# Performance work log

Hardware: AMD Instinct MI355X
Metric: run time of the kernel (lower is better)

The kernel has to match this reference:

```python
import jax, jax.numpy as jnp
import numpy as np

# Sparse MinkUNet-style backbone sizes
N0, N1, N2, N3 = 100000, 50000, 25000, 12500  # voxels per level (batch-concatenated)
K, KD = 27, 8        # 3x3x3 kernel offsets, stride-2 child offsets
B, S = 8, 1024       # batch, seed_num
C0, C1, C2, C3 = 32, 64, 128, 256
COUT = 512


def _w(k, shape, fan_in):
    return jax.random.normal(k, shape, dtype=jnp.float32) / np.sqrt(fan_in)


def setup_inputs() -> dict:
    key = jax.random.key(0)
    ks = jax.random.split(key, 32)
    inp = {}
    inp["feats"] = jax.random.normal(ks[0], (N0, 3), dtype=jnp.float32)
    # neighbor maps (kernel-offset gather indices, as built by a voxel hash map)
    inp["nbr0"] = jax.random.randint(ks[1], (N0, K), 0, N0, dtype=jnp.int32)
    inp["nbr1"] = jax.random.randint(ks[2], (N1, K), 0, N1, dtype=jnp.int32)
    inp["nbr2"] = jax.random.randint(ks[3], (N2, K), 0, N2, dtype=jnp.int32)
    inp["nbr3"] = jax.random.randint(ks[4], (N3, K), 0, N3, dtype=jnp.int32)
    # stride-2 downsample maps (coarse voxel -> fine children)
    inp["down1"] = jax.random.randint(ks[5], (N1, KD), 0, N0, dtype=jnp.int32)
    inp["down2"] = jax.random.randint(ks[6], (N2, KD), 0, N1, dtype=jnp.int32)
    inp["down3"] = jax.random.randint(ks[7], (N3, KD), 0, N2, dtype=jnp.int32)
    # nearest-parent upsample maps (fine voxel -> coarse parent)
    inp["up2"] = jax.random.randint(ks[8], (N2,), 0, N3, dtype=jnp.int32)
    inp["up1"] = jax.random.randint(ks[9], (N1,), 0, N2, dtype=jnp.int32)
    inp["up0"] = jax.random.randint(ks[10], (N0,), 0, N1, dtype=jnp.int32)
    # nearest-voxel devoxelize index for each FPS seed point
    inp["seed_idx"] = jax.random.randint(ks[11], (B, S), 0, N0, dtype=jnp.int32)
    # conv kernels [K, Cin, Cout] and 1x1 (linear) decoder weights
    inp["W_stem"] = _w(ks[12], (K, 3, C0), K * 3)
    inp["W_b0"] = _w(ks[13], (K, C0, C0), K * C0)
    inp["W_d1"] = _w(ks[14], (KD, C0, C1), KD * C0)
    inp["W_b1"] = _w(ks[15], (K, C1, C1), K * C1)
    inp["W_d2"] = _w(ks[16], (KD, C1, C2), KD * C1)
    inp["W_b2"] = _w(ks[17], (K, C2, C2), K * C2)
    inp["W_d3"] = _w(ks[18], (KD, C2, C3), KD * C2)
    inp["W_b3"] = _w(ks[19], (K, C3, C3), K * C3)
    inp["W_u2"] = _w(ks[20], (C3 + C2, 256), C3 + C2)
    inp["W_u1"] = _w(ks[21], (256 + C1, 128), 256 + C1)
    inp["W_u0"] = _w(ks[22], (128 + C0, 96), 128 + C0)
    inp["W_out"] = _w(ks[23], (96, COUT), 96)
    return inp


def sp_conv(f, nbr, W):
    # gather neighbor features then contract over (kernel offset, in-channel)
    g = f[nbr]                                # [N, K, Cin]
    return jnp.einsum('nkc,kco->no', g, W)    # [N, Cout]


def reference(feats, nbr0, nbr1, nbr2, nbr3, down1, down2, down3,
              up2, up1, up0, seed_idx,
              W_stem, W_b0, W_d1, W_b1, W_d2, W_b2, W_d3, W_b3,
              W_u2, W_u1, W_u0, W_out):
    relu = jax.nn.relu
    # encoder
    x0 = relu(sp_conv(feats, nbr0, W_stem))          # [N0, 32]
    x0 = x0 + relu(sp_conv(x0, nbr0, W_b0))
    x1 = relu(sp_conv(x0, down1, W_d1))              # [N1, 64]
    x1 = x1 + relu(sp_conv(x1, nbr1, W_b1))
    x2 = relu(sp_conv(x1, down2, W_d2))              # [N2, 128]
    x2 = x2 + relu(sp_conv(x2, nbr2, W_b2))
    x3 = relu(sp_conv(x2, down3, W_d3))              # [N3, 256]
    x3 = x3 + relu(sp_conv(x3, nbr3, W_b3))
    # decoder: nearest-parent upsample + skip concat + 1x1 conv
    u2 = relu(jnp.concatenate([x3[up2], x2], axis=-1) @ W_u2)   # [N2, 256]
    u1 = relu(jnp.concatenate([u2[up1], x1], axis=-1) @ W_u1)   # [N1, 128]
    u0 = relu(jnp.concatenate([u1[up0], x0], axis=-1) @ W_u0)   # [N0, 96]
    out_vox = u0 @ W_out                                        # [N0, 512]
    seed_feats = out_vox[seed_idx]                              # [B, S, 512]
    return jnp.transpose(seed_feats, (0, 2, 1))                 # [B, 512, S]
```

## Files before the change

kernel.cpp:

```cpp
#include <hip/hip_runtime.h>

typedef unsigned short u16;
typedef unsigned int u32;
typedef __bf16 bf16x8 __attribute__((ext_vector_type(8)));
typedef float f32x4 __attribute__((ext_vector_type(4)));
typedef u16 u16x4 __attribute__((ext_vector_type(4)));

#define NV0 100000
#define NV1 50000
#define NV2 25000
#define NV3 12500

enum : long {
  OFF_WB0  = 0,
  OFF_WD1  = 27648,
  OFF_WB1  = 44032,
  OFF_WD2  = 154624,
  OFF_WB2  = 220160,
  OFF_WD3  = 662528,
  OFF_WB3  = 924672,
  OFF_WU2  = 2694144,
  OFF_WU1  = 2792448,
  OFF_WU0  = 2833408,
  OFF_WOUT = 2848768,
  OFF_TA   = 2897920,
  OFF_X0   = OFF_TA  + 3200000,
  OFF_X1   = OFF_X0  + 3200000,
  OFF_X2   = OFF_X1  + 3200000,
  OFF_X3   = OFF_X2  + 3200000,
  OFF_U2   = OFF_X3  + 3200000,
  OFF_U1   = OFF_U2  + 6400000,
  OFF_U0S  = OFF_U1  + 6400000,
  OFF_END  = OFF_U0S + 786432,
};

__device__ __forceinline__ float b2f(u16 u) {
  union { u32 i; float f; } x; x.i = ((u32)u) << 16; return x.f;
}
__device__ __forceinline__ u16 f2b(float f) {
  union { float f; u32 i; } x; x.f = f;
  u32 r = (x.i + 0x7FFFu + ((x.i >> 16) & 1u)) >> 16;
  return (u16)r;
}
__device__ __forceinline__ void gload16(const u16* g, const u16* l) {
  __builtin_amdgcn_global_load_lds(
      (const __attribute__((address_space(1))) void*)g,
      (__attribute__((address_space(3))) void*)(u16*)l, 16, 0, 0);
}
__device__ __forceinline__ void store_out(u16* p, float v)  { *p = f2b(v); }
__device__ __forceinline__ void store_out(float* p, float v) { *p = v; }
constexpr int ilog2c(int x) { return x <= 1 ? 0 : 1 + ilog2c(x / 2); }

struct PD { const float* src; u16* dst; int KK, CIN, COUT; };
struct PrepArgs { PD d[11]; };

__global__ __launch_bounds__(256) void prep_k(PrepArgs pa) {
  const PD d = pa.d[blockIdx.y];
  const int cc = d.CIN * d.COUT;
  const int total = d.KK * cc;
  for (int e = blockIdx.x * 256 + threadIdx.x; e < total; e += gridDim.x * 256) {
    int k = e / cc;
    int r = e - k * cc;
    int c = r / d.COUT;
    int o = r - c * d.COUT;
    d.dst[(k * d.COUT + o) * d.CIN + c] = f2b(d.src[e]);
  }
}

__global__ __launch_bounds__(256) void stem_k(const float* __restrict__ feats,
                                              const int* __restrict__ nbr0,
                                              const float* __restrict__ wstem,
                                              u16* __restrict__ out) {
  __shared__ float Wl[27 * 3 * 32];
  const int tid = threadIdx.x;
  for (int i = tid; i < 2592; i += 256) Wl[i] = wstem[i];
  __syncthreads();
  const int n = blockIdx.x * 8 + (tid >> 5);
  const int o = tid & 31;
  if (n >= NV0) return;
  float acc = 0.f;
  const int* nb = nbr0 + n * 27;
  #pragma unroll
  for (int k = 0; k < 27; k++) {
    const int iv = nb[k];
    const float* f = feats + iv * 3;
    acc = fmaf(f[0], Wl[(k * 3 + 0) * 32 + o], acc);
    acc = fmaf(f[1], Wl[(k * 3 + 1) * 32 + o], acc);
    acc = fmaf(f[2], Wl[(k * 3 + 2) * 32 + o], acc);
  }
  out[n * 32 + o] = f2b(fmaxf(acc, 0.f));
}

template <int BM, int BN, int WM, int WN, int COUTF, int KCT, int BK, int MODE,
          int CIN, int KK, int KSP, int CA, bool RES, bool DORELU, bool PARTIAL,
          int MINW, typename OT>
__global__ __launch_bounds__(256, MINW) void gemm_k(
    const u16* __restrict__ src0, const u16* __restrict__ src1,
    const int* __restrict__ idx0, const int* __restrict__ idx1,
    const u16* __restrict__ wt, const u16* __restrict__ base,
    OT* __restrict__ out, int N) {
  constexpr int NWM = BM / WM, NWN = BN / WN;
  static_assert(NWM * NWN == 4, "4 waves");
  static_assert(BK == 32 || BK == 64, "BK 32/64");
  constexpr int MI = WM / 16, NI = WN / 16;
  constexpr int CB = KCT - CA;
  constexpr int SLOTS = BK / 8;
  constexpr int RPC = 64 / SLOTS;
  constexpr int LRPC = ilog2c(RPC);
  constexpr int ACH = (BM * BK) / 512;
  constexpr int BCH = (BN * BK) / 512;
  constexpr int LOGC = ilog2c(CIN);
  constexpr int LBM = ilog2c(BM);
  constexpr int NIDX = (MODE == 0) ? BM * KSP : (MODE == 1 ? BM : (MODE == 2 ? 2 * BM : 1));
  static_assert(KCT % BK == 0, "K mult of BK");
  static_assert(MODE != 1 || (CA % BK == 0), "concat boundary aligned");

  __shared__ u16 As[2][BM * BK];
  __shared__ u16 Bs[2][BN * BK];
  __shared__ int Is[NIDX];
  const int tid = threadIdx.x;
  const int w = tid >> 6, lane = tid & 63;
  const int quad = lane >> 4, l16 = lane & 15;
  const int wm = w % NWM, wn = w / NWM;
  const int row0 = blockIdx.x * BM;
  const int col0 = blockIdx.y * BN;
  const int Nm1 = N - 1;
  const int k0 = (MODE == 0) ? (int)blockIdx.z * KSP : 0;
  const int k1 = (MODE == 0) ? ((k0 + KSP > KK) ? KK : k0 + KSP) : 0;
  const int kcb = (MODE == 0) ? k0 * CIN : 0;
  const int kce = (MODE == 0) ? k1 * CIN : KCT;
  if constexpr (PARTIAL) out += (long)blockIdx.z * N * COUTF;
  int srow, cl;
  if constexpr (SLOTS == 4) {
    const int p = lane & 7, li = (lane >> 3) & 7;
    srow = (li << 1) | (p >> 2);
    cl   = (((p & 3) ^ (li & 3)) << 3);
  } else {
    srow = lane >> 3;
    cl   = ((lane & 7) ^ (srow & 7)) * 8;
  }

  if constexpr (MODE == 0) {
    const int kcnt = k1 - k0;
    for (int e = tid; e < kcnt * BM; e += 256) {
      const int kl = e >> LBM, r = e & (BM - 1);
      int n = row0 + r; n = (n > Nm1) ? Nm1 : n;
      Is[e] = idx0[(long)n * KK + k0 + kl];
    }
  } else if constexpr (MODE == 1) {
    for (int e = tid; e < BM; e += 256) {
      int n = row0 + e; n = (n > Nm1) ? Nm1 : n;
      Is[e] = idx0[n];
    }
  } else if constexpr (MODE == 2) {
    for (int e = tid; e < BM; e += 256) {
      int n = row0 + e; n = (n > Nm1) ? Nm1 : n;
      const int s = idx0[n];
      Is[e] = idx1[s];
      Is[BM + e] = s;
    }
  }
  if constexpr (MODE != 3) __syncthreads();

  f32x4 acc[MI][NI];
  #pragma unroll
  for (int i = 0; i < MI; i++)
    #pragma unroll
    for (int j = 0; j < NI; j++) acc[i][j] = {0.f, 0.f, 0.f, 0.f};

  auto stage = [&](int buf, int kc0) {
    for (int c = w; c < ACH + BCH; c += 4) {
      const int cab = kc0 + cl;
      if (c < ACH) {
        const int r = (c << LRPC) + srow;
        const u16* gp;
        if constexpr (MODE == 0) {
          const int k = cab >> LOGC;
          gp = src0 + (long)Is[((k - k0) << LBM) | r] * CIN + (cab & (CIN - 1));
        } else if constexpr (MODE == 1) {
          if (kc0 < CA) gp = src0 + (long)Is[r] * CA + cab;
          else {
            int n = row0 + r; n = (n > Nm1) ? Nm1 : n;
            gp = src1 + (long)n * CB + (cab - CA);
          }
        } else if constexpr (MODE == 2) {
          if (kc0 < CA) gp = src0 + (long)Is[r] * CA + cab;
          else          gp = src1 + (long)Is[BM + r] * CB + (cab - CA);
        } else {
          int n = row0 + r; n = (n > Nm1) ? Nm1 : n;
          gp = src0 + (long)n * KCT + cab;
        }
        gload16(gp, &As[buf][c * 512]);
      } else {
        const int cb = c - ACH;
        const int o = col0 + (cb << LRPC) + srow;
        const u16* gp;
        if constexpr (MODE == 0) {
          const int k = cab >> LOGC;
          gp = wt + ((long)(k * COUTF + o)) * CIN + (cab & (CIN - 1));
        } else {
          gp = wt + (long)o * KCT + cab;
        }
        gload16(gp, &Bs[buf][cb * 512]);
      }
    }
  };

  auto faddr = [&](int row, int kk) -> int {
    if constexpr (SLOTS == 4)
      return ((row >> 1) << 6) + ((((row & 1) << 2) + (((row >> 1) & 3) ^ quad)) << 3);
    else
      return (row << 6) + (((((kk << 2) + quad)) ^ (row & 7)) << 3);
  };

  const int nit = (kce - kcb) / BK;
  stage(0, kcb);
  #pragma unroll 1
  for (int it = 0; it < nit; it++) {
    __syncthreads();
    if (it + 1 < nit) stage((it + 1) & 1, kcb + (it + 1) * BK);
    const int buf = it & 1;
    #pragma unroll
    for (int kk = 0; kk < BK / 32; kk++) {
      bf16x8 af[MI], bfr[NI];
      #pragma unroll
      for (int i = 0; i < MI; i++)
        af[i] = *(const bf16x8*)&As[buf][faddr(wm * WM + i * 16 + l16, kk)];
      #pragma unroll
      for (int j = 0; j < NI; j++)
        bfr[j] = *(const bf16x8*)&Bs[buf][faddr(wn * WN + j * 16 + l16, kk)];
      #pragma unroll
      for (int i = 0; i < MI; i++)
        #pragma unroll
        for (int j = 0; j < NI; j++)
          acc[i][j] = __builtin_amdgcn_mfma_f32_16x16x32_bf16(af[i], bfr[j], acc[i][j], 0, 0, 0);
    }
  }

  #pragma unroll
  for (int i = 0; i < MI; i++) {
    #pragma unroll
    for (int j = 0; j < NI; j++) {
      const int col = col0 + wn * WN + j * 16 + l16;
      #pragma unroll
      for (int r = 0; r < 4; r++) {
        const int n = row0 + wm * WM + i * 16 + quad * 4 + r;
        if (n < N) {
          float v = acc[i][j][r];
          if constexpr (RES)         v = b2f(base[(long)n * COUTF + col]) + fmaxf(v, 0.f);
          else if constexpr (DORELU) v = fmaxf(v, 0.f);
          store_out(&out[(long)n * COUTF + col], v);
        }
      }
    }
  }
}

__global__ __launch_bounds__(256) void comb_k(const float* __restrict__ P,
                                              const u16* __restrict__ base,
                                              u16* __restrict__ out, int total) {
  const int i = (blockIdx.x * 256 + threadIdx.x) * 4;
  if (i >= total) return;
  const f32x4 a = *(const f32x4*)&P[i];
  const f32x4 b = *(const f32x4*)&P[total + i];
  u16x4 o;
  #pragma unroll
  for (int j = 0; j < 4; j++)
    o[j] = f2b(b2f(base[i + j]) + fmaxf(a[j] + b[j], 0.f));
  *(u16x4*)&out[i] = o;
}

__global__ __launch_bounds__(256) void tout_k(const float* __restrict__ tmp,
                                              float* __restrict__ outp) {
  __shared__ float tl[64][65];
  const int tid = threadIdx.x;
  const int r0 = blockIdx.x * 64, o0 = blockIdx.y * 64;
  {
    const int rl = tid >> 2, oc = (tid & 3) * 16;
    const float* src = &tmp[(r0 + rl) * 512 + o0 + oc];
    #pragma unroll
    for (int j = 0; j < 16; j++) tl[rl][oc + j] = src[j];
  }
  __syncthreads();
  {
    const int ol = tid >> 2, sc = (tid & 3) * 16;
    const int b = r0 >> 10, s0 = r0 & 1023;
    float* dst = &outp[((long)b * 512 + (o0 + ol)) * 1024 + s0 + sc];
    #pragma unroll
    for (int j = 0; j < 16; j++) dst[j] = tl[sc + j][ol];
  }
}

extern "C" void kernel_launch(void* const* d_in, const int* in_sizes, int n_in,
                              void* d_out, int out_size, void* d_ws, size_t ws_size,
                              hipStream_t stream) {
  const float* feats = (const float*)d_in[0];
  const int* nbr0  = (const int*)d_in[1];
  const int* nbr1  = (const int*)d_in[2];
  const int* nbr2  = (const int*)d_in[3];
  const int* nbr3  = (const int*)d_in[4];
  const int* down1 = (const int*)d_in[5];
  const int* down2 = (const int*)d_in[6];
  const int* down3 = (const int*)d_in[7];
  const int* up2   = (const int*)d_in[8];
  const int* up1   = (const int*)d_in[9];
  const int* up0   = (const int*)d_in[10];
  const int* seed  = (const int*)d_in[11];
  u16* ws = (u16*)d_ws;

  PrepArgs pa;
  pa.d[0]  = {(const float*)d_in[13], ws + OFF_WB0,  27, 32, 32};
  pa.d[1]  = {(const float*)d_in[14], ws + OFF_WD1,  8,  32, 64};
  pa.d[2]  = {(const float*)d_in[15], ws + OFF_WB1,  27, 64, 64};
  pa.d[3]  = {(const float*)d_in[16], ws + OFF_WD2,  8,  64, 128};
  pa.d[4]  = {(const float*)d_in[17], ws + OFF_WB2,  27, 128, 128};
  pa.d[5]  = {(const float*)d_in[18], ws + OFF_WD3,  8,  128, 256};
  pa.d[6]  = {(const float*)d_in[19], ws + OFF_WB3,  27, 256, 256};
  pa.d[7]  = {(const float*)d_in[20], ws + OFF_WU2,  1,  384, 256};
  pa.d[8]  = {(const float*)d_in[21], ws + OFF_WU1,  1,  320, 128};
  pa.d[9]  = {(const float*)d_in[22], ws + OFF_WU0,  1,  160, 96};
  pa.d[10] = {(const float*)d_in[23], ws + OFF_WOUT, 1,  96,  512};
  prep_k<<<dim3(128, 11), 256, 0, stream>>>(pa);

  u16* ta  = ws + OFF_TA;
  u16* x0  = ws + OFF_X0;
  u16* x1  = ws + OFF_X1;
  u16* x2  = ws + OFF_X2;
  u16* x3  = ws + OFF_X3;
  u16* u2b = ws + OFF_U2;
  u16* u1b = ws + OFF_U1;
  u16* u0s = ws + OFF_U0S;
  float* P   = (float*)(ws + OFF_U2);
  float* tmp = (float*)(ws + OFF_TA);

  stem_k<<<12500, 256, 0, stream>>>(feats, nbr0, (const float*)d_in[12], ta);

  gemm_k<128, 32, 32, 32, 32, 864, 32, 0, 32, 27, 27, 0, true, true, false, 4, u16>
      <<<dim3(782, 1, 1), 256, 0, stream>>>(ta, nullptr, nbr0, nullptr, ws + OFF_WB0, ta, x0, NV0);
  gemm_k<64, 64, 32, 32, 64, 256, 64, 0, 32, 8, 8, 0, false, true, false, 4, u16>
      <<<dim3(782, 1, 1), 256, 0, stream>>>(x0, nullptr, down1, nullptr, ws + OFF_WD1, nullptr, ta, NV1);
  gemm_k<64, 64, 32, 32, 64, 1728, 64, 0, 64, 27, 27, 0, true, true, false, 4, u16>
      <<<dim3(782, 1, 1), 256, 0, stream>>>(ta, nullptr, nbr1, nullptr, ws + OFF_WB1, ta, x1, NV1);
  gemm_k<64, 128, 32, 64, 128, 512, 64, 0, 64, 8, 8, 0, false, true, false, 3, u16>
      <<<dim3(391, 1, 1), 256, 0, stream>>>(x1, nullptr, down2, nullptr, ws + OFF_WD2, nullptr, ta, NV2);
  gemm_k<64, 128, 32, 64, 128, 3456, 64, 0, 128, 27, 14, 0, false, false, true, 3, float>
      <<<dim3(391, 1, 2), 256, 0, stream>>>(ta, nullptr, nbr2, nullptr, ws + OFF_WB2, nullptr, P, NV2);
  comb_k<<<dim3(3125), 256, 0, stream>>>(P, ta, x2, NV2 * 128);
  gemm_k<64, 128, 32, 64, 256, 1024, 64, 0, 128, 8, 8, 0, false, true, false, 3, u16>
      <<<dim3(196, 2, 1), 256, 0, stream>>>(x2, nullptr, down3, nullptr, ws + OFF_WD3, nullptr, ta, NV3);
  gemm_k<64, 128, 32, 64, 256, 6912, 64, 0, 256, 27, 14, 0, false, false, true, 3, float>
      <<<dim3(196, 2, 2), 256, 0, stream>>>(ta, nullptr, nbr3, nullptr, ws + OFF_WB3, nullptr, P, NV3);
  comb_k<<<dim3(3125), 256, 0, stream>>>(P, ta, x3, NV3 * 256);
  gemm_k<64, 128, 32, 64, 256, 384, 64, 1, 32, 1, 1, 256, false, true, false, 3, u16>
      <<<dim3(391, 2, 1), 256, 0, stream>>>(x3, x2, up2, nullptr, ws + OFF_WU2, nullptr, u2b, NV2);
  gemm_k<64, 128, 32, 64, 128, 320, 64, 1, 32, 1, 1, 256, false, true, false, 3, u16>
      <<<dim3(782, 1, 1), 256, 0, stream>>>(u2b, x1, up1, nullptr, ws + OFF_WU1, nullptr, u1b, NV1);
  gemm_k<64, 96, 32, 48, 96, 160, 32, 2, 32, 1, 1, 128, false, true, false, 4, u16>
      <<<dim3(128, 1, 1), 256, 0, stream>>>(u1b, x0, seed, up0, ws + OFF_WU0, nullptr, u0s, 8192);
  gemm_k<64, 128, 32, 64, 512, 96, 32, 3, 32, 1, 1, 0, false, false, false, 4, float>
      <<<dim3(128, 4, 1), 256, 0, stream>>>(u0s, nullptr, nullptr, nullptr, ws + OFF_WOUT, nullptr, tmp, 8192);
  tout_k<<<dim3(128, 8), 256, 0, stream>>>(tmp, (float*)d_out);
}
```

Baseline: 543.3 us.

## Add triple-buffered async LDS pipeline with explicit vmcnt waits to gather GEMMs

Adds a PIPE template mode to the gather GEMM kernel that uses three LDS buffers, prefetching two K-steps ahead with direct-to-LDS loads and raw s_barrier plus explicit s_waitcnt vmcnt counts. The intent is to hide global gather latency behind MFMA compute instead of fully draining loads at each __syncthreads. Most conv and decoder GEMMs switch to this path, and their min-waves launch bound is lowered, which costs more LDS and may reduce occupancy. The fixed vmcnt counts assume each wave issues a uniform number of chunk loads per stage.

```diff
diff --git a/kernel.cpp b/kernel.cpp
--- a/kernel.cpp
+++ b/kernel.cpp
@@ -47,6 +47,14 @@
       (const __attribute__((address_space(1))) void*)g,
       (__attribute__((address_space(3))) void*)(u16*)l, 16, 0, 0);
 }
+template <int N> __device__ __forceinline__ void waitvm() {
+  asm volatile("s_waitcnt vmcnt(%0)" :: "i"(N) : "memory");
+}
+__device__ __forceinline__ void rbar() {
+  asm volatile("" ::: "memory");
+  __builtin_amdgcn_s_barrier();
+  asm volatile("" ::: "memory");
+}
 __device__ __forceinline__ void store_out(u16* p, float v)  { *p = f2b(v); }
 __device__ __forceinline__ void store_out(float* p, float v) { *p = v; }
 constexpr int ilog2c(int x) { return x <= 1 ? 0 : 1 + ilog2c(x / 2); }
@@ -93,7 +101,7 @@
 
 template <int BM, int BN, int WM, int WN, int COUTF, int KCT, int BK, int MODE,
           int CIN, int KK, int KSP, int CA, bool RES, bool DORELU, bool PARTIAL,
-          int MINW, typename OT>
+          bool PIPE, int MINW, typename OT>
 __global__ __launch_bounds__(256, MINW) void gemm_k(
     const u16* __restrict__ src0, const u16* __restrict__ src1,
     const int* __restrict__ idx0, const int* __restrict__ idx1,
@@ -112,11 +120,14 @@
   constexpr int LOGC = ilog2c(CIN);
   constexpr int LBM = ilog2c(BM);
   constexpr int NIDX = (MODE == 0) ? BM * KSP : (MODE == 1 ? BM : (MODE == 2 ? 2 * BM : 1));
+  constexpr int NBUF = PIPE ? 3 : 2;
+  static_assert(!PIPE || ((ACH + BCH) % 4 == 0), "uniform chunks per wave for PIPE");
+  constexpr int CH1 = (ACH + BCH) / 4;
   static_assert(KCT % BK == 0, "K mult of BK");
   static_assert(MODE != 1 || (CA % BK == 0), "concat boundary aligned");
 
-  __shared__ u16 As[2][BM * BK];
-  __shared__ u16 Bs[2][BN * BK];
+  __shared__ u16 As[NBUF][BM * BK];
+  __shared__ u16 Bs[NBUF][BN * BK];
   __shared__ int Is[NIDX];
   const int tid = threadIdx.x;
   const int w = tid >> 6, lane = tid & 63;
@@ -213,13 +224,7 @@
       return (row << 6) + (((((kk << 2) + quad)) ^ (row & 7)) << 3);
   };
 
-  const int nit = (kce - kcb) / BK;
-  stage(0, kcb);
-  #pragma unroll 1
-  for (int it = 0; it < nit; it++) {
-    __syncthreads();
-    if (it + 1 < nit) stage((it + 1) & 1, kcb + (it + 1) * BK);
-    const int buf = it & 1;
+  auto compute = [&](int buf) {
     #pragma unroll
     for (int kk = 0; kk < BK / 32; kk++) {
       bf16x8 af[MI], bfr[NI];
@@ -234,6 +239,36 @@
         #pragma unroll
         for (int j = 0; j < NI; j++)
           acc[i][j] = __builtin_amdgcn_mfma_f32_16x16x32_bf16(af[i], bfr[j], acc[i][j], 0, 0, 0);
+    }
+  };
+
+  const int nit = (kce - kcb) / BK;
+  if constexpr (PIPE) {
+    stage(0, kcb);
+    if (nit > 1) stage(1, kcb + BK);
+    int cur = 0;
+    #pragma unroll 1
+    for (int it = 0; it < nit; it++) {
+      rbar();
+      if (it + 2 < nit) {
+        int nb = cur + 2; if (nb >= 3) nb -= 3;
+        stage(nb, kcb + (it + 2) * BK);
+      }
+      const int rem = nit - 1 - it;
+      if (rem >= 2)      waitvm<2 * CH1>();
+      else if (rem == 1) waitvm<CH1>();
+      else               waitvm<0>();
+      rbar();
+      compute(cur);
+      cur++; if (cur == 3) cur = 0;
+    }
+  } else {
+    stage(0, kcb);
+    #pragma unroll 1
+    for (int it = 0; it < nit; it++) {
+      __syncthreads();
+      if (it + 1 < nit) stage((it + 1) & 1, kcb + (it + 1) * BK);
+      compute(it & 1);
     }
   }
 
@@ -335,29 +370,29 @@
 
   stem_k<<<12500, 256, 0, stream>>>(feats, nbr0, (const float*)d_in[12], ta);
 
-  gemm_k<128, 32, 32, 32, 32, 864, 32, 0, 32, 27, 27, 0, true, true, false, 4, u16>
+  gemm_k<128, 32, 32, 32, 32, 864, 32, 0, 32, 27, 27, 0, true, true, false, false, 4, u16>
       <<<dim3(782, 1, 1), 256, 0, stream>>>(ta, nullptr, nbr0, nullptr, ws + OFF_WB0, ta, x0, NV0);
-  gemm_k<64, 64, 32, 32, 64, 256, 64, 0, 32, 8, 8, 0, false, true, false, 4, u16>
+  gemm_k<64, 64, 32, 32, 64, 256, 64, 0, 32, 8, 8, 0, false, true, false, true, 3, u16>
       <<<dim3(782, 1, 1), 256, 0, stream>>>(x0, nullptr, down1, nullptr, ws + OFF_WD1, nullptr, ta, NV1);
-  gemm_k<64, 64, 32, 32, 64, 1728, 64, 0, 64, 27, 27, 0, true, true, false, 4, u16>
+  gemm_k<64, 64, 32, 32, 64, 1728, 64, 0, 64, 27, 27, 0, true, true, false, true, 2, u16>
       <<<dim3(782, 1, 1), 256, 0, stream>>>(ta, nullptr, nbr1, nullptr, ws + OFF_WB1, ta, x1, NV1);
-  gemm_k<64, 128, 32, 64, 128, 512, 64, 0, 64, 8, 8, 0, false, true, false, 3, u16>
+  gemm_k<64, 128, 32, 64, 128, 512, 64, 0, 64, 8, 8, 0, false, true, false, true, 2, u16>
       <<<dim3(391, 1, 1), 256, 0, stream>>>(x1, nullptr, down2, nullptr, ws + OFF_WD2, nullptr, ta, NV2);
-  gemm_k<64, 128, 32, 64, 128, 3456, 64, 0, 128, 27, 14, 0, false, false, true, 3, float>
+  gemm_k<64, 128, 32, 64, 128, 3456, 64, 0, 128, 27, 14, 0, false, false, true, true, 2, float>
       <<<dim3(391, 1, 2), 256, 0, stream>>>(ta, nullptr, nbr2, nullptr, ws + OFF_WB2, nullptr, P, NV2);
   comb_k<<<dim3(3125), 256, 0, stream>>>(P, ta, x2, NV2 * 128);
-  gemm_k<64, 128, 32, 64, 256, 1024, 64, 0, 128, 8, 8, 0, false, true, false, 3, u16>
+  gemm_k<64, 128, 32, 64, 256, 1024, 64, 0, 128, 8, 8, 0, false, true, false, true, 2, u16>
       <<<dim3(196, 2, 1), 256, 0, stream>>>(x2, nullptr, down3, nullptr, ws + OFF_WD3, nullptr, ta, NV3);
-  gemm_k<64, 128, 32, 64, 256, 6912, 64, 0, 256, 27, 14, 0, false, false, true, 3, float>
+  gemm_k<64, 128, 32, 64, 256, 6912, 64, 0, 256, 27, 14, 0, false, false, true, true, 2, float>
       <<<dim3(196, 2, 2), 256, 0, stream>>>(ta, nullptr, nbr3, nullptr, ws + OFF_WB3, nullptr, P, NV3);
   comb_k<<<dim3(3125), 256, 0, stream>>>(P, ta, x3, NV3 * 256);
-  gemm_k<64, 128, 32, 64, 256, 384, 64, 1, 32, 1, 1, 256, false, true, false, 3, u16>
+  gemm_k<64, 128, 32, 64, 256, 384, 64, 1, 32, 1, 1, 256, false, true, false, true, 2, u16>
       <<<dim3(391, 2, 1), 256, 0, stream>>>(x3, x2, up2, nullptr, ws + OFF_WU2, nullptr, u2b, NV2);
-  gemm_k<64, 128, 32, 64, 128, 320, 64, 1, 32, 1, 1, 256, false, true, false, 3, u16>
+  gemm_k<64, 128, 32, 64, 128, 320, 64, 1, 32, 1, 1, 256, false, true, false, true, 2, u16>
       <<<dim3(782, 1, 1), 256, 0, stream>>>(u2b, x1, up1, nullptr, ws + OFF_WU1, nullptr, u1b, NV1);
-  gemm_k<64, 96, 32, 48, 96, 160, 32, 2, 32, 1, 1, 128, false, true, false, 4, u16>
+  gemm_k<64, 96, 32, 48, 96, 160, 32, 2, 32, 1, 1, 128, false, true, false, false, 4, u16>
       <<<dim3(128, 1, 1), 256, 0, stream>>>(u1b, x0, seed, up0, ws + OFF_WU0, nullptr, u0s, 8192);
-  gemm_k<64, 128, 32, 64, 512, 96, 32, 3, 32, 1, 1, 0, false, false, false, 4, float>
+  gemm_k<64, 128, 32, 64, 512, 96, 32, 3, 32, 1, 1, 0, false, false, false, true, 4, float>
       <<<dim3(128, 4, 1), 256, 0, stream>>>(u0s, nullptr, nullptr, nullptr, ws + OFF_WOUT, nullptr, tmp, 8192);
   tout_k<<<dim3(128, 8), 256, 0, stream>>>(tmp, (float*)d_out);
 }
```

Result: slower. 573.1 us (+5.5%).

## Partition sparse-conv gathers by source-row halves to improve cache locality

Applied to the files above, without the earlier changes.

Each sparse convolution and downsample layer now runs two grid slices. Each slice gathers only neighbour rows whose index falls in its half of the source array and substitutes a shared zero row for the rest. The partial float results are then summed by a combine kernel that applies the ReLU and the residual. The aim is to halve the working set each slice touches so random gathers hit in cache more often. The cost is doubled MFMA work, extra float partial traffic, extra combine launches, and the deeper layers being split into two accumulating launches over kernel offsets with larger tiles.

```diff
diff --git a/kernel.cpp b/kernel.cpp
--- a/kernel.cpp
+++ b/kernel.cpp
@@ -31,7 +31,8 @@
   OFF_U2   = OFF_X3  + 3200000,
   OFF_U1   = OFF_U2  + 6400000,
   OFF_U0S  = OFF_U1  + 6400000,
-  OFF_END  = OFF_U0S + 786432,
+  OFF_ZERO = OFF_U0S + 786432,
+  OFF_END  = OFF_ZERO + 256,
 };
 
 __device__ __forceinline__ float b2f(u16 u) {
@@ -52,9 +53,10 @@
 constexpr int ilog2c(int x) { return x <= 1 ? 0 : 1 + ilog2c(x / 2); }
 
 struct PD { const float* src; u16* dst; int KK, CIN, COUT; };
-struct PrepArgs { PD d[11]; };
+struct PrepArgs { PD d[11]; u16* zrow; };
 
 __global__ __launch_bounds__(256) void prep_k(PrepArgs pa) {
+  if (blockIdx.y == 0 && blockIdx.x == 0) pa.zrow[threadIdx.x] = 0;
   const PD d = pa.d[blockIdx.y];
   const int cc = d.CIN * d.COUT;
   const int total = d.KK * cc;
@@ -93,15 +95,18 @@
 
 template <int BM, int BN, int WM, int WN, int COUTF, int KCT, int BK, int MODE,
           int CIN, int KK, int KSP, int CA, bool RES, bool DORELU, bool PARTIAL,
-          int MINW, typename OT>
+          bool IDXS, bool ACC, int MINW, typename OT>
 __global__ __launch_bounds__(256, MINW) void gemm_k(
     const u16* __restrict__ src0, const u16* __restrict__ src1,
     const int* __restrict__ idx0, const int* __restrict__ idx1,
     const u16* __restrict__ wt, const u16* __restrict__ base,
-    OT* __restrict__ out, int N) {
+    const u16* __restrict__ zrow,
+    OT* __restrict__ out, int N, int k0r, int k1r, int nsrc) {
   constexpr int NWM = BM / WM, NWN = BN / WN;
   static_assert(NWM * NWN == 4, "4 waves");
   static_assert(BK == 32 || BK == 64, "BK 32/64");
+  static_assert(!IDXS || MODE == 0, "IDXS only for sparse conv");
+  static_assert(!ACC || PARTIAL, "ACC implies PARTIAL");
   constexpr int MI = WM / 16, NI = WN / 16;
   constexpr int CB = KCT - CA;
   constexpr int SLOTS = BK / 8;
@@ -125,10 +130,10 @@
   const int row0 = blockIdx.x * BM;
   const int col0 = blockIdx.y * BN;
   const int Nm1 = N - 1;
-  const int k0 = (MODE == 0) ? (int)blockIdx.z * KSP : 0;
-  const int k1 = (MODE == 0) ? ((k0 + KSP > KK) ? KK : k0 + KSP) : 0;
-  const int kcb = (MODE == 0) ? k0 * CIN : 0;
-  const int kce = (MODE == 0) ? k1 * CIN : KCT;
+  const int kcb = (MODE == 0) ? k0r * CIN : 0;
+  const int kce = (MODE == 0) ? k1r * CIN : KCT;
+  const int half = IDXS ? (nsrc >> 1) : 0;
+  const int lo   = IDXS ? (int)blockIdx.z * half : 0;
   if constexpr (PARTIAL) out += (long)blockIdx.z * N * COUTF;
   int srow, cl;
   if constexpr (SLOTS == 4) {
@@ -141,11 +146,11 @@
   }
 
   if constexpr (MODE == 0) {
-    const int kcnt = k1 - k0;
+    const int kcnt = k1r - k0r;
     for (int e = tid; e < kcnt * BM; e += 256) {
       const int kl = e >> LBM, r = e & (BM - 1);
       int n = row0 + r; n = (n > Nm1) ? Nm1 : n;
-      Is[e] = idx0[(long)n * KK + k0 + kl];
+      Is[e] = idx0[(long)n * KK + k0r + kl];
     }
   } else if constexpr (MODE == 1) {
     for (int e = tid; e < BM; e += 256) {
@@ -176,7 +181,14 @@
         const u16* gp;
         if constexpr (MODE == 0) {
           const int k = cab >> LOGC;
-          gp = src0 + (long)Is[((k - k0) << LBM) | r] * CIN + (cab & (CIN - 1));
+          const int i = Is[((k - k0r) << LBM) | r];
+          if constexpr (IDXS) {
+            gp = ((u32)(i - lo) < (u32)half)
+                   ? src0 + (long)i * CIN + (cab & (CIN - 1))
+                   : zrow;
+          } else {
+            gp = src0 + (long)i * CIN + (cab & (CIN - 1));
+          }
         } else if constexpr (MODE == 1) {
           if (kc0 < CA) gp = src0 + (long)Is[r] * CA + cab;
           else {
@@ -247,15 +259,22 @@
         const int n = row0 + wm * WM + i * 16 + quad * 4 + r;
         if (n < N) {
           float v = acc[i][j][r];
-          if constexpr (RES)         v = b2f(base[(long)n * COUTF + col]) + fmaxf(v, 0.f);
-          else if constexpr (DORELU) v = fmaxf(v, 0.f);
-          store_out(&out[(long)n * COUTF + col], v);
+          const long ofs = (long)n * COUTF + col;
+          if constexpr (PARTIAL) {
+            if constexpr (ACC) v += (float)out[ofs];
+          } else if constexpr (RES) {
+            v = b2f(base[ofs]) + fmaxf(v, 0.f);
+          } else if constexpr (DORELU) {
+            v = fmaxf(v, 0.f);
+          }
+          store_out(&out[ofs], v);
         }
       }
     }
   }
 }
 
+template <bool WB>
 __global__ __launch_bounds__(256) void comb_k(const float* __restrict__ P,
                                               const u16* __restrict__ base,
                                               u16* __restrict__ out, int total) {
@@ -265,8 +284,11 @@
   const f32x4 b = *(const f32x4*)&P[total + i];
   u16x4 o;
   #pragma unroll
-  for (int j = 0; j < 4; j++)
-    o[j] = f2b(b2f(base[i + j]) + fmaxf(a[j] + b[j], 0.f));
+  for (int j = 0; j < 4; j++) {
+    float v = fmaxf(a[j] + b[j], 0.f);
+    if constexpr (WB) v = b2f(base[i + j]) + v;
+    o[j] = f2b(v);
+  }
   *(u16x4*)&out[i] = o;
 }
 
@@ -308,6 +330,7 @@
   const int* seed  = (const int*)d_in[11];
   u16* ws = (u16*)d_ws;
 
+  u16* zrow = ws + OFF_ZERO;
   PrepArgs pa;
   pa.d[0]  = {(const float*)d_in[13], ws + OFF_WB0,  27, 32, 32};
   pa.d[1]  = {(const float*)d_in[14], ws + OFF_WD1,  8,  32, 64};
@@ -320,6 +343,7 @@
   pa.d[8]  = {(const float*)d_in[21], ws + OFF_WU1,  1,  320, 128};
   pa.d[9]  = {(const float*)d_in[22], ws + OFF_WU0,  1,  160, 96};
   pa.d[10] = {(const float*)d_in[23], ws + OFF_WOUT, 1,  96,  512};
+  pa.zrow  = zrow;
   prep_k<<<dim3(128, 11), 256, 0, stream>>>(pa);
 
   u16* ta  = ws + OFF_TA;
@@ -335,29 +359,38 @@
 
   stem_k<<<12500, 256, 0, stream>>>(feats, nbr0, (const float*)d_in[12], ta);
 
-  gemm_k<128, 32, 32, 32, 32, 864, 32, 0, 32, 27, 27, 0, true, true, false, 4, u16>
-      <<<dim3(782, 1, 1), 256, 0, stream>>>(ta, nullptr, nbr0, nullptr, ws + OFF_WB0, ta, x0, NV0);
-  gemm_k<64, 64, 32, 32, 64, 256, 64, 0, 32, 8, 8, 0, false, true, false, 4, u16>
-      <<<dim3(782, 1, 1), 256, 0, stream>>>(x0, nullptr, down1, nullptr, ws + OFF_WD1, nullptr, ta, NV1);
-  gemm_k<64, 64, 32, 32, 64, 1728, 64, 0, 64, 27, 27, 0, true, true, false, 4, u16>
-      <<<dim3(782, 1, 1), 256, 0, stream>>>(ta, nullptr, nbr1, nullptr, ws + OFF_WB1, ta, x1, NV1);
-  gemm_k<64, 128, 32, 64, 128, 512, 64, 0, 64, 8, 8, 0, false, true, false, 3, u16>
-      <<<dim3(391, 1, 1), 256, 0, stream>>>(x1, nullptr, down2, nullptr, ws + OFF_WD2, nullptr, ta, NV2);
-  gemm_k<64, 128, 32, 64, 128, 3456, 64, 0, 128, 27, 14, 0, false, false, true, 3, float>
-      <<<dim3(391, 1, 2), 256, 0, stream>>>(ta, nullptr, nbr2, nullptr, ws + OFF_WB2, nullptr, P, NV2);
-  comb_k<<<dim3(3125), 256, 0, stream>>>(P, ta, x2, NV2 * 128);
-  gemm_k<64, 128, 32, 64, 256, 1024, 64, 0, 128, 8, 8, 0, false, true, false, 3, u16>
-      <<<dim3(196, 2, 1), 256, 0, stream>>>(x2, nullptr, down3, nullptr, ws + OFF_WD3, nullptr, ta, NV3);
-  gemm_k<64, 128, 32, 64, 256, 6912, 64, 0, 256, 27, 14, 0, false, false, true, 3, float>
-      <<<dim3(196, 2, 2), 256, 0, stream>>>(ta, nullptr, nbr3, nullptr, ws + OFF_WB3, nullptr, P, NV3);
-  comb_k<<<dim3(3125), 256, 0, stream>>>(P, ta, x3, NV3 * 256);
-  gemm_k<64, 128, 32, 64, 256, 384, 64, 1, 32, 1, 1, 256, false, true, false, 3, u16>
-      <<<dim3(391, 2, 1), 256, 0, stream>>>(x3, x2, up2, nullptr, ws + OFF_WU2, nullptr, u2b, NV2);
-  gemm_k<64, 128, 32, 64, 128, 320, 64, 1, 32, 1, 1, 256, false, true, false, 3, u16>
-      <<<dim3(782, 1, 1), 256, 0, stream>>>(u2b, x1, up1, nullptr, ws + OFF_WU1, nullptr, u1b, NV1);
-  gemm_k<64, 96, 32, 48, 96, 160, 32, 2, 32, 1, 1, 128, false, true, false, 4, u16>
-      <<<dim3(128, 1, 1), 256, 0, stream>>>(u1b, x0, seed, up0, ws + OFF_WU0, nullptr, u0s, 8192);
-  gemm_k<64, 128, 32, 64, 512, 96, 32, 3, 32, 1, 1, 0, false, false, false, 4, float>
-      <<<dim3(128, 4, 1), 256, 0, stream>>>(u0s, nullptr, nullptr, nullptr, ws + OFF_WOUT, nullptr, tmp, 8192);
+  gemm_k<128, 32, 32, 32, 32, 864, 32, 0, 32, 27, 27, 0, false, false, true, true, false, 4, float>
+      <<<dim3(782, 1, 2), 256, 0, stream>>>(ta, nullptr, nbr0, nullptr, ws + OFF_WB0, nullptr, zrow, P, NV0, 0, 27, NV0);
+  comb_k<true><<<3125, 256, 0, stream>>>(P, ta, x0, NV0 * 32);
+  gemm_k<64, 64, 32, 32, 64, 256, 64, 0, 32, 8, 8, 0, false, false, true, true, false, 4, float>
+      <<<dim3(782, 1, 2), 256, 0, stream>>>(x0, nullptr, down1, nullptr, ws + OFF_WD1, nullptr, zrow, P, NV1, 0, 8, NV0);
+  comb_k<false><<<3125, 256, 0, stream>>>(P, x0, ta, NV1 * 64);
+  gemm_k<64, 64, 32, 32, 64, 1728, 64, 0, 64, 27, 27, 0, false, false, true, true, false, 4, float>
+      <<<dim3(782, 1, 2), 256, 0, stream>>>(ta, nullptr, nbr1, nullptr, ws + OFF_WB1, nullptr, zrow, P, NV1, 0, 27, NV1);
+  comb_k<true><<<3125, 256, 0, stream>>>(P, ta, x1, NV1 * 64);
+  gemm_k<64, 128, 32, 64, 128, 512, 64, 0, 64, 8, 8, 0, false, false, true, true, false, 3, float>
+      <<<dim3(391, 1, 2), 256, 0, stream>>>(x1, nullptr, down2, nullptr, ws + OFF_WD2, nullptr, zrow, P, NV2, 0, 8, NV1);
+  comb_k<false><<<3125, 256, 0, stream>>>(P, x1, ta, NV2 * 128);
+  gemm_k<128, 128, 64, 64, 128, 3456, 64, 0, 128, 27, 14, 0, false, false, true, true, false, 2, float>
+      <<<dim3(196, 1, 2), 256, 0, stream>>>(ta, nullptr, nbr2, nullptr, ws + OFF_WB2, nullptr, zrow, P, NV2, 0, 14, NV2);
+  gemm_k<128, 128, 64, 64, 128, 3456, 64, 0, 128, 27, 14, 0, false, false, true, true, true, 2, float>
+      <<<dim3(196, 1, 2), 256, 0, stream>>>(ta, nullptr, nbr2, nullptr, ws + OFF_WB2, nullptr, zrow, P, NV2, 14, 27, NV2);
+  comb_k<true><<<3125, 256, 0, stream>>>(P, ta, x2, NV2 * 128);
+  gemm_k<64, 128, 32, 64, 256, 1024, 64, 0, 128, 8, 8, 0, false, false, true, true, false, 3, float>
+      <<<dim3(196, 2, 2), 256, 0, stream>>>(x2, nullptr, down3, nullptr, ws + OFF_WD3, nullptr, zrow, P, NV3, 0, 8, NV2);
+  comb_k<false><<<3125, 256, 0, stream>>>(P, x2, ta, NV3 * 256);
+  gemm_k<128, 128, 64, 64, 256, 6912, 64, 0, 256, 27, 14, 0, false, false, true, true, false, 2, float>
+      <<<dim3(98, 2, 2), 256, 0, stream>>>(ta, nullptr, nbr3, nullptr, ws + OFF_WB3, nullptr, zrow, P, NV3, 0, 14, NV3);
+  gemm_k<128, 128, 64, 64, 256, 6912, 64, 0, 256, 27, 14, 0, false, false, true, true, true, 2, float>
+      <<<dim3(98, 2, 2), 256, 0, stream>>>(ta, nullptr, nbr3, nullptr, ws + OFF_WB3, nullptr, zrow, P, NV3, 14, 27, NV3);
+  comb_k<true><<<3125, 256, 0, stream>>>(P, ta, x3, NV3 * 256);
+  gemm_k<64, 128, 32, 64, 256, 384, 64, 1, 32, 1, 1, 256, false, true, false, false, false, 3, u16>
+      <<<dim3(391, 2, 1), 256, 0, stream>>>(x3, x2, up2, nullptr, ws + OFF_WU2, nullptr, zrow, u2b, NV2, 0, 0, 0);
+  gemm_k<64, 128, 32, 64, 128, 320, 64, 1, 32, 1, 1, 256, false, true, false, false, false, 3, u16>
+      <<<dim3(782, 1, 1), 256, 0, stream>>>(u2b, x1, up1, nullptr, ws + OFF_WU1, nullptr, zrow, u1b, NV1, 0, 0, 0);
+  gemm_k<64, 96, 32, 48, 96, 160, 32, 2, 32, 1, 1, 128, false, true, false, false, false, 4, u16>
+      <<<dim3(128, 1, 1), 256, 0, stream>>>(u1b, x0, seed, up0, ws + OFF_WU0, nullptr, zrow, u0s, 8192, 0, 0, 0);
+  gemm_k<64, 128, 32, 64, 512, 96, 32, 3, 32, 1, 1, 0, false, false, false, false, false, 4, float>
+      <<<dim3(128, 4, 1), 256, 0, stream>>>(u0s, nullptr, nullptr, nullptr, ws + OFF_WOUT, nullptr, zrow, tmp, 8192, 0, 0, 0);
   tout_k<<<dim3(128, 8), 256, 0, stream>>>(tmp, (float*)d_out);
 }
```

Result: slower. 766.5 us (+41.1%).
